# Kernel tuning notes

Hardware: AMD Instinct MI355X
Metric: run time of the kernel (lower is better)

## Reference

```python
import jax, jax.numpy as jnp
import numpy as np


def setup_inputs() -> dict:
    key = jax.random.key(0)
    k1, k2 = jax.random.split(key)
    B, C, D, H, W = 2, 32, 80, 80, 80
    NC = 28
    feats = jax.random.normal(k1, (B, C, D, H, W), dtype=jnp.float32)
    labels = jax.random.randint(k2, (B, D, H, W), 0, NC, dtype=jnp.int64)
    # hierarchy tree distance matrix: small positive ints, symmetric, zero diagonal
    rng = np.random.default_rng(0)
    dm = rng.integers(1, 9, size=(NC, NC)).astype(np.float32)
    dm = np.maximum(dm, dm.T)
    np.fill_diagonal(dm, 0.0)
    dist_mat = jnp.asarray(dm)
    return {"feats": feats, "dist_mat": dist_mat, "labels": labels, "max_triplet": 200}


def _forward(feats, dist_mat, labels, max_triplet):
    B, C, D, H, W = feats.shape
    NC = dist_mat.shape[0]
    k = int(max_triplet)
    # nearest-resize of labels to feats' spatial shape is identity (same resolution)
    lab = labels.reshape(-1)                       # [N]
    f = jnp.transpose(feats, (0, 2, 3, 4, 1)).reshape(-1, C)  # [N, C]
    N = f.shape[0]
    arangeN = jnp.arange(N, dtype=jnp.int32)
    # which classes exist in this batch (class 0 = background is excluded)
    counts = jnp.zeros((NC,), jnp.int32).at[lab].add(1)
    exist = (counts > 0).at[0].set(False)          # [NC]
    BIG = jnp.float32(1e9)

    def first_k(mask):
        # indices of the first k True positions (in order), plus total count
        cnt = jnp.sum(mask)
        rank = jnp.cumsum(mask) - 1                # rank among True elements
        slot = jnp.where(mask & (rank < k), rank, k)
        buf = jnp.zeros((k + 1,), jnp.int32).at[slot].set(arangeN)
        return buf[:k], cnt

    total = jnp.float32(0.0)
    ccount = jnp.int32(0)
    iota = jnp.arange(k)
    for ii in range(1, NC):
        ad = dist_mat[ii]                           # [NC]
        ad = jnp.where(ad == 0, jnp.float32(256.0), ad)
        ad = jnp.where(exist, ad, BIG)              # restrict to existing classes
        min_dist = jnp.min(ad)
        pos_cls = exist & (ad == min_dist)          # positive classes (closest in tree)
        m_anchor = lab == ii
        m_pos = pos_cls[lab]
        m_neg = (~m_anchor) & (~m_pos) & (lab != 0)
        ia, ca = first_k(m_anchor)
        ip, cp = first_k(m_pos)
        ing, cn = first_k(m_neg)
        min_size = jnp.minimum(jnp.minimum(ca, cp), jnp.minimum(cn, k))
        valid = iota < min_size                     # [k]
        fa, fp, fn = f[ia], f[ip], f[ing]           # [k, C]
        d_pos = dist_mat[ii, lab[ip]]
        d_neg = dist_mat[ii, lab[ing]]
        dpos = 1.0 - jnp.sum(fa * fp, axis=1)       # cosine-style distance
        dneg = 1.0 - jnp.sum(fa * fn, axis=1)
        margin = 0.1 + (d_neg - d_pos) / 8.0
        tl = jax.nn.relu(dpos - dneg + margin) * valid
        has = exist[ii] & (min_size > 0)
        total = total + jnp.where(has, jnp.sum(tl) / jnp.maximum(min_size, 1), 0.0)
        ccount = ccount + has.astype(jnp.int32)

    loss = jnp.where(ccount > 0, total / jnp.maximum(ccount, 1), jnp.float32(0.0))
    return loss


def reference(feats, dist_mat, labels, max_triplet):
    return _forward(feats, dist_mat, labels, max_triplet)
```

## Files before the change

kernel.cpp:

```cpp
#include <hip/hip_runtime.h>

#define SPX  512000
#define NBX  2
#define NCH  32
#define NTOT (NBX*SPX)
#define NCL  28
#define SEG  64
#define TTH  (NTOT/SEG)
#define BS1  64
#define GR1  (TTH/BS1)
#define KCAP 256
#define HS   29

__device__ __forceinline__ int faddr(int n, int c) {
  int b = (n >= SPX) ? 1 : 0;
  int r = n - b * SPX;
  return (b * NCH + c) * SPX + r;
}

__global__ void k_hist(const int* __restrict__ lab, int* __restrict__ hist) {
  __shared__ int h[BS1 * HS];
  const int tid = threadIdx.x;
  const int t = blockIdx.x * BS1 + tid;
  for (int L = 0; L < NCL; ++L) h[tid * HS + L] = 0;
  const int4* p = (const int4*)(lab + t * SEG);
#pragma unroll
  for (int j = 0; j < SEG / 4; ++j) {
    int4 v = p[j];
    ++h[tid * HS + v.x];
    ++h[tid * HS + v.y];
    ++h[tid * HS + v.z];
    ++h[tid * HS + v.w];
  }
  for (int L = 0; L < NCL; ++L) hist[L * TTH + t] = h[tid * HS + L];
}

__global__ void k_scan(int* __restrict__ hist, int* __restrict__ counts) {
  const int L = blockIdx.x;
  int* a = hist + L * TTH;
  __shared__ int s[256];
  const int tid = threadIdx.x;
  const int CH = (TTH + 255) / 256;
  int lo = tid * CH; if (lo > TTH) lo = TTH;
  int hi = lo + CH;  if (hi > TTH) hi = TTH;
  int sum = 0;
  for (int i = lo; i < hi; ++i) sum += a[i];
  s[tid] = sum;
  __syncthreads();
  for (int off = 1; off < 256; off <<= 1) {
    int v = (tid >= off) ? s[tid - off] : 0;
    __syncthreads();
    s[tid] += v;
    __syncthreads();
  }
  if (tid == 255) counts[L] = s[255];
  int run = s[tid] - sum;
  for (int i = lo; i < hi; ++i) { int t0 = a[i]; a[i] = run; run += t0; }
}

__global__ void k_select(const int* __restrict__ lab, const int* __restrict__ P,
                         int* __restrict__ firstk, int* __restrict__ snap,
                         const int* __restrict__ kptr) {
  __shared__ int cur[BS1 * HS];
  const int tid = threadIdx.x;
  const int t = blockIdx.x * BS1 + tid;
  int k = kptr[0]; if (k > KCAP) k = KCAP;
  for (int L = 0; L < NCL; ++L) cur[tid * HS + L] = P[L * TTH + t];
  const int4* p = (const int4*)(lab + t * SEG);
  int n = t * SEG;
  for (int j = 0; j < SEG / 4; ++j) {
    int4 v = p[j];
#pragma unroll
    for (int q = 0; q < 4; ++q) {
      int L = (q == 0) ? v.x : (q == 1) ? v.y : (q == 2) ? v.z : v.w;
      int c = cur[tid * HS + L];
      if (L != 0 && c < k) {
        int slot = L * KCAP + c;
        firstk[slot] = n;
        int* srow = snap + slot * NCL;
        for (int L2 = 0; L2 < NCL; ++L2) srow[L2] = cur[tid * HS + L2];
      }
      cur[tid * HS + L] = c + 1;
      ++n;
    }
  }
}

__global__ void k_main(const float* __restrict__ feats, const float* __restrict__ dm,
                       const int* __restrict__ counts, const int* __restrict__ firstk,
                       const int* __restrict__ snap, const int* __restrict__ kptr,
                       float* __restrict__ perclass) {
  const int ii = blockIdx.x + 1;
  const int tid = threadIdx.x;
  __shared__ int cnt_s[NCL];
  __shared__ unsigned int posmask_s, negmask_s;
  __shared__ int minsize_s, has_s, k_s;
  __shared__ int ipos[KCAP], ineg[KCAP];
  __shared__ float partial[8];

  if (tid < NCL) cnt_s[tid] = counts[tid];
  __syncthreads();

  if (tid == 0) {
    int k = kptr[0]; if (k > KCAP) k = KCAP; if (k < 0) k = 0;
    k_s = k;
    float ad[NCL];
    unsigned em = 0;
    float mind = 1e9f;
    for (int L = 0; L < NCL; ++L) {
      bool ex = (L != 0) && (cnt_s[L] > 0);
      float v = dm[ii * NCL + L];
      if (v == 0.0f) v = 256.0f;
      if (!ex) v = 1e9f;
      ad[L] = v;
      if (ex) em |= 1u << L;
      if (v < mind) mind = v;
    }
    unsigned pm = 0, nm = 0;
    int cp = 0, cn = 0;
    for (int L = 1; L < NCL; ++L) {
      if (((em >> L) & 1) && ad[L] == mind) { pm |= 1u << L; cp += cnt_s[L]; }
    }
    for (int L = 1; L < NCL; ++L) {
      if (L == ii) continue;
      if ((pm >> L) & 1) continue;
      nm |= 1u << L; cn += cnt_s[L];
    }
    int ca = cnt_s[ii];
    int ms = ca; if (cp < ms) ms = cp; if (cn < ms) ms = cn; if (k < ms) ms = k;
    posmask_s = pm; negmask_s = nm; minsize_s = ms;
    has_s = (((em >> ii) & 1) && ms > 0) ? 1 : 0;
  }
  __syncthreads();

  if (!has_s) {
    if (tid == 0) { perclass[2 * (ii - 1)] = 0.f; perclass[2 * (ii - 1) + 1] = 0.f; }
    return;
  }

  const int k = k_s;
  const unsigned pm = posmask_s, nm = negmask_s;

  for (int L = 1; L < NCL; ++L) {
    bool isp = (pm >> L) & 1, isn = (nm >> L) & 1;
    if (!isp && !isn) continue;
    int len = cnt_s[L]; if (len > k) len = k;
    for (int p = tid; p < len; p += 256) {
      const int slot = L * KCAP + p;
      const int x = firstk[slot];
      const int* srow = snap + slot * NCL;
      int pr = 0, nr = 0;
      for (int L2 = 1; L2 < NCL; ++L2) {
        int sv = srow[L2];
        if ((pm >> L2) & 1) pr += sv;
        if ((nm >> L2) & 1) nr += sv;
      }
      int packed = x | (L << 20);
      if (isp && pr < k) ipos[pr] = packed;
      if (isn && nr < k) ineg[nr] = packed;
    }
  }
  __syncthreads();

  const int ms = minsize_s;
  const int grp = tid >> 5, lane = tid & 31;
  float acc = 0.f;
  for (int j = grp; j < ms; j += 8) {
    int na = firstk[ii * KCAP + j];
    int pp = ipos[j], nn = ineg[j];
    int np = pp & 0xFFFFF, lp = pp >> 20;
    int ng = nn & 0xFFFFF, ln = nn >> 20;
    float fa = feats[faddr(na, lane)];
    float fp = feats[faddr(np, lane)];
    float fn = feats[faddr(ng, lane)];
    float sp = fa * fp, sn = fa * fn;
#pragma unroll
    for (int o = 16; o >= 1; o >>= 1) {
      sp += __shfl_xor(sp, o, 64);
      sn += __shfl_xor(sn, o, 64);
    }
    if (lane == 0) {
      float dp = dm[ii * NCL + lp], dn = dm[ii * NCL + ln];
      float tl = sn - sp + 0.1f + (dn - dp) * 0.125f;
      if (tl > 0.f) acc += tl;
    }
  }
  if (lane == 0) partial[grp] = acc;
  __syncthreads();
  if (tid == 0) {
    float s = 0.f;
    for (int g = 0; g < 8; ++g) s += partial[g];
    perclass[2 * (ii - 1)] = s / (float)ms;
    perclass[2 * (ii - 1) + 1] = 1.f;
  }
}

__global__ void k_fin(const float* __restrict__ perclass, float* __restrict__ out) {
  if (threadIdx.x == 0 && blockIdx.x == 0) {
    float tot = 0.f, cc = 0.f;
    for (int i = 0; i < NCL - 1; ++i) { tot += perclass[2 * i]; cc += perclass[2 * i + 1]; }
    out[0] = (cc > 0.f) ? tot / cc : 0.f;
  }
}

extern "C" void kernel_launch(void* const* d_in, const int* in_sizes, int n_in,
                              void* d_out, int out_size, void* d_ws, size_t ws_size,
                              hipStream_t stream) {
  const float* feats = (const float*)d_in[0];
  const float* dm    = (const float*)d_in[1];
  const int*   lab   = (const int*)d_in[2];
  const int*   kptr  = (const int*)d_in[3];
  float* out = (float*)d_out;

  int* hist   = (int*)d_ws;
  int* counts = hist + NCL * TTH;
  int* firstk = counts + NCL;
  int* snap   = firstk + NCL * KCAP;
  float* perclass = (float*)(snap + NCL * KCAP * NCL);

  k_hist  <<<GR1, BS1, 0, stream>>>(lab, hist);
  k_scan  <<<NCL, 256, 0, stream>>>(hist, counts);
  k_select<<<GR1, BS1, 0, stream>>>(lab, hist, firstk, snap, kptr);
  k_main  <<<NCL - 1, 256, 0, stream>>>(feats, dm, counts, firstk, snap, kptr, perclass);
  k_fin   <<<1, 64, 0, stream>>>(perclass, out);
}
```

Measured before the change: 266.5 us.

## Rewrite histogram with wave ballots, prune select threads, fuse final reduction

The histogram now has each wave count label classes with ballot and popcount over coalesced 64-element chunks, replacing per-thread LDS histograms with strided int4 loads. Select threads whose chunk prefix counts already reach k for every class exit early, which skips most of the scan over the label array. Class 0 is dropped from the hist and snap layouts, k_main uses 512 threads, and the final averaging kernel is folded into k_main through a last-block-done atomic counter. The changes cut global memory traffic and one launch, at the cost of 27 ballots per element and extra atomic ordering.

```diff
diff --git a/kernel.cpp b/kernel.cpp
--- a/kernel.cpp
+++ b/kernel.cpp
@@ -5,10 +5,7 @@
 #define NCH  32
 #define NTOT (NBX*SPX)
 #define NCL  28
-#define SEG  64
-#define TTH  (NTOT/SEG)
-#define BS1  64
-#define GR1  (TTH/BS1)
+#define NCHK 16000
 #define KCAP 256
 #define HS   29
 
@@ -18,31 +15,46 @@
   return (b * NCH + c) * SPX + r;
 }
 
-__global__ void k_hist(const int* __restrict__ lab, int* __restrict__ hist) {
-  __shared__ int h[BS1 * HS];
-  const int tid = threadIdx.x;
-  const int t = blockIdx.x * BS1 + tid;
-  for (int L = 0; L < NCL; ++L) h[tid * HS + L] = 0;
-  const int4* p = (const int4*)(lab + t * SEG);
-#pragma unroll
-  for (int j = 0; j < SEG / 4; ++j) {
-    int4 v = p[j];
-    ++h[tid * HS + v.x];
-    ++h[tid * HS + v.y];
-    ++h[tid * HS + v.z];
-    ++h[tid * HS + v.w];
-  }
-  for (int L = 0; L < NCL; ++L) hist[L * TTH + t] = h[tid * HS + L];
-}
-
-__global__ void k_scan(int* __restrict__ hist, int* __restrict__ counts) {
+__global__ __launch_bounds__(256) void k_hist(const int* __restrict__ lab,
+                                              int* __restrict__ hist,
+                                              int* __restrict__ done) {
+  const int tid = threadIdx.x;
+  const int lane = tid & 63;
+  const int wave = (blockIdx.x << 2) + (tid >> 6);
+  const int base = wave << 4;
+  if (blockIdx.x == 0 && tid == 0)
+    __hip_atomic_store(done, 0, __ATOMIC_RELAXED, __HIP_MEMORY_SCOPE_AGENT);
+
+  int c[16];
+#pragma unroll
+  for (int i = 0; i < 16; ++i) {
+    int v = lab[(base + i) * 64 + lane];
+    int cnt = 0;
+#pragma unroll
+    for (int L = 1; L < NCL; ++L) {
+      unsigned long long m = __ballot(v == L);
+      int pop = __popcll(m);
+      cnt = (lane == L) ? pop : cnt;
+    }
+    c[i] = cnt;
+  }
+  if (lane >= 1 && lane < NCL) {
+    int4* row = (int4*)(hist + (lane - 1) * NCHK + base);
+    row[0] = make_int4(c[0],  c[1],  c[2],  c[3]);
+    row[1] = make_int4(c[4],  c[5],  c[6],  c[7]);
+    row[2] = make_int4(c[8],  c[9],  c[10], c[11]);
+    row[3] = make_int4(c[12], c[13], c[14], c[15]);
+  }
+}
+
+__global__ __launch_bounds__(256) void k_scan(int* __restrict__ hist, int* __restrict__ counts) {
   const int L = blockIdx.x;
-  int* a = hist + L * TTH;
+  int* a = hist + L * NCHK;
   __shared__ int s[256];
   const int tid = threadIdx.x;
-  const int CH = (TTH + 255) / 256;
-  int lo = tid * CH; if (lo > TTH) lo = TTH;
-  int hi = lo + CH;  if (hi > TTH) hi = TTH;
+  const int CH = 63;
+  int lo = tid * CH; if (lo > NCHK) lo = NCHK;
+  int hi = lo + CH;  if (hi > NCHK) hi = NCHK;
   int sum = 0;
   for (int i = lo; i < hi; ++i) sum += a[i];
   s[tid] = sum;
@@ -53,50 +65,71 @@
     s[tid] += v;
     __syncthreads();
   }
-  if (tid == 255) counts[L] = s[255];
+  if (tid == 255) counts[L + 1] = s[255];
+  if (tid == 0 && L == 0) counts[0] = 0;
   int run = s[tid] - sum;
   for (int i = lo; i < hi; ++i) { int t0 = a[i]; a[i] = run; run += t0; }
 }
 
-__global__ void k_select(const int* __restrict__ lab, const int* __restrict__ P,
-                         int* __restrict__ firstk, int* __restrict__ snap,
-                         const int* __restrict__ kptr) {
-  __shared__ int cur[BS1 * HS];
-  const int tid = threadIdx.x;
-  const int t = blockIdx.x * BS1 + tid;
+__global__ __launch_bounds__(256) void k_select(const int* __restrict__ lab,
+                                                const int* __restrict__ P,
+                                                int* __restrict__ firstk,
+                                                int* __restrict__ snap,
+                                                const int* __restrict__ kptr) {
+  __shared__ int cur[256 * HS];
+  const int tid = threadIdx.x;
+  const int tt = blockIdx.x * 256 + tid;
+  if (tt >= NCHK) return;
   int k = kptr[0]; if (k > KCAP) k = KCAP;
-  for (int L = 0; L < NCL; ++L) cur[tid * HS + L] = P[L * TTH + t];
-  const int4* p = (const int4*)(lab + t * SEG);
-  int n = t * SEG;
-  for (int j = 0; j < SEG / 4; ++j) {
-    int4 v = p[j];
+  const int row = tid * HS;
+  int mn = 0x7fffffff;
+#pragma unroll
+  for (int L = 1; L < NCL; ++L) {
+    int v = P[(L - 1) * NCHK + tt];
+    cur[row + L] = v;
+    mn = min(mn, v);
+  }
+  if (mn >= k) return;
+
+  const int4* p4 = (const int4*)(lab + tt * 64);
+  int n = tt * 64;
+  for (int j = 0; j < 16; ++j) {
+    int4 v = p4[j];
 #pragma unroll
     for (int q = 0; q < 4; ++q) {
       int L = (q == 0) ? v.x : (q == 1) ? v.y : (q == 2) ? v.z : v.w;
-      int c = cur[tid * HS + L];
-      if (L != 0 && c < k) {
-        int slot = L * KCAP + c;
-        firstk[slot] = n;
-        int* srow = snap + slot * NCL;
-        for (int L2 = 0; L2 < NCL; ++L2) srow[L2] = cur[tid * HS + L2];
-      }
-      cur[tid * HS + L] = c + 1;
+      if (L != 0) {
+        int c = cur[row + L];
+        if (c < k) {
+          int slot = (L - 1) * KCAP + c;
+          firstk[slot] = n;
+          int* srow = snap + slot * 27;
+#pragma unroll
+          for (int L2 = 1; L2 < NCL; ++L2) srow[L2 - 1] = cur[row + L2];
+        }
+        cur[row + L] = c + 1;
+      }
       ++n;
     }
   }
 }
 
-__global__ void k_main(const float* __restrict__ feats, const float* __restrict__ dm,
-                       const int* __restrict__ counts, const int* __restrict__ firstk,
-                       const int* __restrict__ snap, const int* __restrict__ kptr,
-                       float* __restrict__ perclass) {
+__global__ __launch_bounds__(512) void k_main(const float* __restrict__ feats,
+                                              const float* __restrict__ dm,
+                                              const int* __restrict__ counts,
+                                              const int* __restrict__ firstk,
+                                              const int* __restrict__ snap,
+                                              const int* __restrict__ kptr,
+                                              float* __restrict__ perclass,
+                                              int* __restrict__ done,
+                                              float* __restrict__ out) {
   const int ii = blockIdx.x + 1;
   const int tid = threadIdx.x;
   __shared__ int cnt_s[NCL];
   __shared__ unsigned int posmask_s, negmask_s;
   __shared__ int minsize_s, has_s, k_s;
   __shared__ int ipos[KCAP], ineg[KCAP];
-  __shared__ float partial[8];
+  __shared__ float partial[16];
 
   if (tid < NCL) cnt_s[tid] = counts[tid];
   __syncthreads();
@@ -118,9 +151,8 @@
     }
     unsigned pm = 0, nm = 0;
     int cp = 0, cn = 0;
-    for (int L = 1; L < NCL; ++L) {
+    for (int L = 1; L < NCL; ++L)
       if (((em >> L) & 1) && ad[L] == mind) { pm |= 1u << L; cp += cnt_s[L]; }
-    }
     for (int L = 1; L < NCL; ++L) {
       if (L == ii) continue;
       if ((pm >> L) & 1) continue;
@@ -133,73 +165,79 @@
   }
   __syncthreads();
 
-  if (!has_s) {
-    if (tid == 0) { perclass[2 * (ii - 1)] = 0.f; perclass[2 * (ii - 1) + 1] = 0.f; }
-    return;
-  }
-
-  const int k = k_s;
-  const unsigned pm = posmask_s, nm = negmask_s;
-
-  for (int L = 1; L < NCL; ++L) {
-    bool isp = (pm >> L) & 1, isn = (nm >> L) & 1;
-    if (!isp && !isn) continue;
-    int len = cnt_s[L]; if (len > k) len = k;
-    for (int p = tid; p < len; p += 256) {
-      const int slot = L * KCAP + p;
-      const int x = firstk[slot];
-      const int* srow = snap + slot * NCL;
-      int pr = 0, nr = 0;
-      for (int L2 = 1; L2 < NCL; ++L2) {
-        int sv = srow[L2];
-        if ((pm >> L2) & 1) pr += sv;
-        if ((nm >> L2) & 1) nr += sv;
-      }
-      int packed = x | (L << 20);
-      if (isp && pr < k) ipos[pr] = packed;
-      if (isn && nr < k) ineg[nr] = packed;
-    }
-  }
-  __syncthreads();
-
-  const int ms = minsize_s;
-  const int grp = tid >> 5, lane = tid & 31;
-  float acc = 0.f;
-  for (int j = grp; j < ms; j += 8) {
-    int na = firstk[ii * KCAP + j];
-    int pp = ipos[j], nn = ineg[j];
-    int np = pp & 0xFFFFF, lp = pp >> 20;
-    int ng = nn & 0xFFFFF, ln = nn >> 20;
-    float fa = feats[faddr(na, lane)];
-    float fp = feats[faddr(np, lane)];
-    float fn = feats[faddr(ng, lane)];
-    float sp = fa * fp, sn = fa * fn;
-#pragma unroll
-    for (int o = 16; o >= 1; o >>= 1) {
-      sp += __shfl_xor(sp, o, 64);
-      sn += __shfl_xor(sn, o, 64);
-    }
-    if (lane == 0) {
-      float dp = dm[ii * NCL + lp], dn = dm[ii * NCL + ln];
-      float tl = sn - sp + 0.1f + (dn - dp) * 0.125f;
-      if (tl > 0.f) acc += tl;
-    }
-  }
-  if (lane == 0) partial[grp] = acc;
-  __syncthreads();
+  float result = 0.f, hasf = 0.f;
+  if (has_s) {
+    const int k = k_s;
+    const unsigned pm = posmask_s, nm = negmask_s;
+
+    for (int L = 1; L < NCL; ++L) {
+      bool isp = (pm >> L) & 1, isn = (nm >> L) & 1;
+      if (!isp && !isn) continue;
+      int len = cnt_s[L]; if (len > k) len = k;
+      for (int p = tid; p < len; p += 512) {
+        const int slot = (L - 1) * KCAP + p;
+        const int x = firstk[slot];
+        const int* srow = snap + slot * 27;
+        int pr = 0, nr = 0;
+#pragma unroll
+        for (int L2 = 1; L2 < NCL; ++L2) {
+          int sv = srow[L2 - 1];
+          if ((pm >> L2) & 1) pr += sv;
+          if ((nm >> L2) & 1) nr += sv;
+        }
+        int packed = x | (L << 20);
+        if (isp && pr < k) ipos[pr] = packed;
+        if (isn && nr < k) ineg[nr] = packed;
+      }
+    }
+    __syncthreads();
+
+    const int ms = minsize_s;
+    const int grp = tid >> 5, lane = tid & 31;
+    float acc = 0.f;
+#pragma unroll 2
+    for (int j = grp; j < ms; j += 16) {
+      int na = firstk[(ii - 1) * KCAP + j];
+      int pp = ipos[j], nn = ineg[j];
+      int np = pp & 0xFFFFF, lp = pp >> 20;
+      int ng = nn & 0xFFFFF, ln = nn >> 20;
+      float fa = feats[faddr(na, lane)];
+      float fp = feats[faddr(np, lane)];
+      float fn = feats[faddr(ng, lane)];
+      float sp = fa * fp, sn = fa * fn;
+#pragma unroll
+      for (int o = 16; o >= 1; o >>= 1) {
+        sp += __shfl_xor(sp, o, 64);
+        sn += __shfl_xor(sn, o, 64);
+      }
+      if (lane == 0) {
+        float dp = dm[ii * NCL + lp], dn = dm[ii * NCL + ln];
+        float tl = sn - sp + 0.1f + (dn - dp) * 0.125f;
+        if (tl > 0.f) acc += tl;
+      }
+    }
+    if (lane == 0) partial[grp] = acc;
+    __syncthreads();
+    if (tid == 0) {
+      float s = 0.f;
+      for (int g = 0; g < 16; ++g) s += partial[g];
+      result = s / (float)minsize_s;
+      hasf = 1.f;
+    }
+  }
+
   if (tid == 0) {
-    float s = 0.f;
-    for (int g = 0; g < 8; ++g) s += partial[g];
-    perclass[2 * (ii - 1)] = s / (float)ms;
-    perclass[2 * (ii - 1) + 1] = 1.f;
-  }
-}
-
-__global__ void k_fin(const float* __restrict__ perclass, float* __restrict__ out) {
-  if (threadIdx.x == 0 && blockIdx.x == 0) {
-    float tot = 0.f, cc = 0.f;
-    for (int i = 0; i < NCL - 1; ++i) { tot += perclass[2 * i]; cc += perclass[2 * i + 1]; }
-    out[0] = (cc > 0.f) ? tot / cc : 0.f;
+    __hip_atomic_store(&perclass[2 * (ii - 1)],     result, __ATOMIC_RELAXED, __HIP_MEMORY_SCOPE_AGENT);
+    __hip_atomic_store(&perclass[2 * (ii - 1) + 1], hasf,   __ATOMIC_RELAXED, __HIP_MEMORY_SCOPE_AGENT);
+    int prev = __hip_atomic_fetch_add(done, 1, __ATOMIC_ACQ_REL, __HIP_MEMORY_SCOPE_AGENT);
+    if (prev == (NCL - 1) - 1) {
+      float tot = 0.f, cc = 0.f;
+      for (int i = 0; i < NCL - 1; ++i) {
+        tot += __hip_atomic_load(&perclass[2 * i],     __ATOMIC_RELAXED, __HIP_MEMORY_SCOPE_AGENT);
+        cc  += __hip_atomic_load(&perclass[2 * i + 1], __ATOMIC_RELAXED, __HIP_MEMORY_SCOPE_AGENT);
+      }
+      out[0] = (cc > 0.f) ? tot / cc : 0.f;
+    }
   }
 }
 
@@ -213,14 +251,15 @@
   float* out = (float*)d_out;
 
   int* hist   = (int*)d_ws;
-  int* counts = hist + NCL * TTH;
+  int* counts = hist + 27 * NCHK;
   int* firstk = counts + NCL;
-  int* snap   = firstk + NCL * KCAP;
-  float* perclass = (float*)(snap + NCL * KCAP * NCL);
-
-  k_hist  <<<GR1, BS1, 0, stream>>>(lab, hist);
-  k_scan  <<<NCL, 256, 0, stream>>>(hist, counts);
-  k_select<<<GR1, BS1, 0, stream>>>(lab, hist, firstk, snap, kptr);
-  k_main  <<<NCL - 1, 256, 0, stream>>>(feats, dm, counts, firstk, snap, kptr, perclass);
-  k_fin   <<<1, 64, 0, stream>>>(perclass, out);
-}
+  int* snap   = firstk + 27 * KCAP;
+  int* done   = snap + 27 * KCAP * 27;
+  float* perclass = (float*)(done + 4);
+
+  k_hist  <<<250, 256, 0, stream>>>(lab, hist, done);
+  k_scan  <<<NCL - 1, 256, 0, stream>>>(hist, counts);
+  k_select<<<63, 256, 0, stream>>>(lab, hist, firstk, snap, kptr);
+  k_main  <<<NCL - 1, 512, 0, stream>>>(feats, dm, counts, firstk, snap, kptr,
+                                        perclass, done, out);
+}
```

Result: slower. 273.4 us (+2.6%).
